# Kernel optimization log

Measured on AMD Instinct MI355X. Metric: run time of the kernel, lower is better.

## Reference

```python
import jax, jax.numpy as jnp
import numpy as np

N = 16384      # number of points (pixels)
C = 64         # value channels of U
D_REF = 5      # bilateral reference feature dim (xy + rgb)


def setup_inputs() -> dict:
    key = jax.random.key(0)
    k1, k2 = jax.random.split(key)
    U = jax.random.normal(k1, (N, C), dtype=jnp.float32)
    ref = jax.random.normal(k2, (N, D_REF), dtype=jnp.float32)
    return {"U": U, "ref": ref}


def reference(U, ref):
    # Gaussian filtering on reference features (exact form of the LSH-approx filter):
    #   out[i] = sum_j exp(-0.5 * ||ref_i - ref_j||^2) * U[j]  -  U[i]
    sq = jnp.sum(ref * ref, axis=-1)                      # [N]
    d2 = sq[:, None] + sq[None, :] - 2.0 * (ref @ ref.T)  # [N, N] squared distances
    K = jnp.exp(-0.5 * jnp.maximum(d2, 0.0))              # [N, N] Gaussian kernel
    return K @ U - U                                       # [N, C]
```

## Files before the change

### kernel.cpp

```cpp
#include <hip/hip_runtime.h>
#include <hip/hip_bf16.h>
#include <stdint.h>

#define N_PTS 16384
#define C_CH  64
#define D_REF 5
#define LOG2E 1.44269504088896340736f
#define IBLOCKS 64

typedef __attribute__((ext_vector_type(8))) short bf16x8;
typedef __attribute__((ext_vector_type(4))) float f32x4;

__device__ __forceinline__ unsigned short bf16rn(float v) {
    unsigned u = __builtin_bit_cast(unsigned, v) + 0x8000u;
    return (unsigned short)(u >> 16);
}
__device__ __forceinline__ float bf16tof(unsigned short h) {
    unsigned u = ((unsigned)h) << 16;
    return __builtin_bit_cast(float, u);
}
__device__ __forceinline__ unsigned pack2bf16(float lo, float hi) {
    unsigned a = __builtin_bit_cast(unsigned, lo) + 0x8000u;
    unsigned b = __builtin_bit_cast(unsigned, hi) + 0x8000u;
    return __builtin_amdgcn_perm(b, a, 0x07060302u);
}
__device__ __forceinline__ float fast_exp2(float x) {
#if __has_builtin(__builtin_amdgcn_exp2f)
    return __builtin_amdgcn_exp2f(x);
#else
    return exp2f(x);
#endif
}

__global__ __launch_bounds__(256) void prep_all(
    const float* __restrict__ U, const float* __restrict__ ref,
    unsigned short* __restrict__ packA, unsigned short* __restrict__ packB,
    unsigned short* __restrict__ utPack)
{
    __shared__ unsigned short tile[64 * 80];
    const int bid = blockIdx.x;
    const int t   = threadIdx.x;

    if (bid < 512) {
        const int gid  = bid * 256 + t;
        const int half = gid >> 16;
        const int id   = gid & 0xFFFF;
        const int tile16 = id >> 6;
        const int lane = id & 63;
        const int q    = lane >> 4;
        const int m    = lane & 15;
        const int p = half ? (tile16 * 16 + m)
                           : ((tile16 >> 1) * 32 + (m >> 2) * 8 + (m & 3) + (tile16 & 1) * 4);

        const float* r = ref + (size_t)p * D_REF;
        float rv[5];
        float sq = 0.f;
#pragma unroll
        for (int d = 0; d < 5; ++d) { rv[d] = r[d]; sq += rv[d] * rv[d]; }
        const float h = -0.5f * LOG2E * sq;

        unsigned short bh[5], bl[5];
#pragma unroll
        for (int d = 0; d < 5; ++d) {
            const float base = half ? rv[d] * LOG2E : rv[d];
            bh[d] = bf16rn(base);
            bl[d] = bf16rn(base - bf16tof(bh[d]));
        }
        const unsigned short hh  = bf16rn(h);
        const unsigned short hl  = bf16rn(h - bf16tof(hh));
        const unsigned short one = 0x3F80;

        unsigned short outv[8];
#pragma unroll
        for (int tt = 0; tt < 8; ++tt) {
            const int k = q * 8 + tt;
            unsigned short v = 0;
            if (!half) {
                if      (k < 5)   v = bh[k];
                else if (k < 10)  v = bh[k - 5];
                else if (k < 15)  v = bl[k - 10];
                else if (k == 15) v = hh;
                else if (k == 16) v = hl;
                else if (k <= 18) v = one;
            } else {
                if      (k < 5)   v = bh[k];
                else if (k < 10)  v = bl[k - 5];
                else if (k < 15)  v = bh[k - 10];
                else if (k <= 16) v = one;
                else if (k == 17) v = hh;
                else if (k == 18) v = hl;
            }
            outv[tt] = v;
        }
        unsigned short* dst = (half ? packB : packA) + ((size_t)tile16 * 64 + lane) * 8;
        *(uint4*)dst = *(uint4*)outv;
    } else {
        const int b  = bid - 512;
        const int j0 = b * 64;
        const int c  = t & 63;
        const int jb = t >> 6;
#pragma unroll
        for (int k = 0; k < 16; ++k) {
            const int jr = jb + k * 4;
            tile[c * 80 + jr] = bf16rn(U[(size_t)(j0 + jr) * C_CH + c]);
        }
        __syncthreads();
#pragma unroll
        for (int rep = 0; rep < 2; ++rep) {
            const int id   = rep * 256 + t;
            const int lane = id & 63;
            const int ct   = (id >> 6) & 3;
            const int kt   = id >> 8;
            const int m    = lane & 15;
            const int q    = lane >> 4;
            const int cc   = ct * 16 + m;
            const int jloc = kt * 32 + q * 8;
            const uint4 frag = *(const uint4*)&tile[cc * 80 + jloc];
            const int jtile  = b * 2 + kt;
            *(uint4*)&utPack[(((size_t)jtile * 4 + ct) * 64 + lane) * 8] = frag;
        }
    }
}

template<int JS>
__global__ __launch_bounds__(256, 4) void lsh_main(
    const float* __restrict__ U,
    const unsigned short* __restrict__ packA,
    const unsigned short* __restrict__ packB,
    const unsigned short* __restrict__ utPack,
    float* __restrict__ part,
    float* __restrict__ out,
    int use_part)
{
    constexpr int UNITS = (N_PTS / JS) / 32;

    const int t    = threadIdx.x;
    const int lane = t & 63;
    const int wave = t >> 6;
    const int q    = lane >> 4;
    const int m    = lane & 15;

    const int ib = blockIdx.x / JS;
    const int js = blockIdx.x % JS;

    bf16x8 bfrag[4];
#pragma unroll
    for (int s = 0; s < 4; ++s) {
        const int itile = ib * 16 + wave * 4 + s;
        bfrag[s] = *(const bf16x8*)(packB + ((size_t)itile * 64 + lane) * 8);
    }

    f32x4 acc[4][4];
#pragma unroll
    for (int s = 0; s < 4; ++s)
#pragma unroll
        for (int ct = 0; ct < 4; ++ct) acc[s][ct] = (f32x4){0.f, 0.f, 0.f, 0.f};

    const unsigned short* pA = packA  + ((size_t)js * UNITS) * 1024 + lane * 8;
    const unsigned short* pU = utPack + ((size_t)js * UNITS) * 2048 + lane * 8;

    bf16x8 ga0 = *(const bf16x8*)pA;
    bf16x8 ga1 = *(const bf16x8*)(pA + 512);

    for (int u = 0; u < UNITS; ++u) {
        bf16x8 nga0 = ga0, nga1 = ga1;
        if (u + 1 < UNITS) {
            nga0 = *(const bf16x8*)(pA + 1024);
            nga1 = *(const bf16x8*)(pA + 1536);
        }

        const f32x4 z = (f32x4){0.f, 0.f, 0.f, 0.f};
        bf16x8 sfrag[4];
#pragma unroll
        for (int sp = 0; sp < 2; ++sp) {
            f32x4 g0a = __builtin_amdgcn_mfma_f32_16x16x32_bf16(ga0, bfrag[sp*2+0], z, 0, 0, 0);
            f32x4 g1a = __builtin_amdgcn_mfma_f32_16x16x32_bf16(ga1, bfrag[sp*2+0], z, 0, 0, 0);
            f32x4 g0b = __builtin_amdgcn_mfma_f32_16x16x32_bf16(ga0, bfrag[sp*2+1], z, 0, 0, 0);
            f32x4 g1b = __builtin_amdgcn_mfma_f32_16x16x32_bf16(ga1, bfrag[sp*2+1], z, 0, 0, 0);
            union { unsigned u[4]; bf16x8 v; } sa, sb;
            sa.u[0] = pack2bf16(fast_exp2(g0a[0]), fast_exp2(g0a[1]));
            sa.u[1] = pack2bf16(fast_exp2(g0a[2]), fast_exp2(g0a[3]));
            sa.u[2] = pack2bf16(fast_exp2(g1a[0]), fast_exp2(g1a[1]));
            sa.u[3] = pack2bf16(fast_exp2(g1a[2]), fast_exp2(g1a[3]));
            sb.u[0] = pack2bf16(fast_exp2(g0b[0]), fast_exp2(g0b[1]));
            sb.u[1] = pack2bf16(fast_exp2(g0b[2]), fast_exp2(g0b[3]));
            sb.u[2] = pack2bf16(fast_exp2(g1b[0]), fast_exp2(g1b[1]));
            sb.u[3] = pack2bf16(fast_exp2(g1b[2]), fast_exp2(g1b[3]));
            sfrag[sp*2+0] = sa.v;
            sfrag[sp*2+1] = sb.v;
        }
#pragma unroll
        for (int ct = 0; ct < 4; ++ct) {
            const bf16x8 uf = *(const bf16x8*)(pU + ct * 512);
#pragma unroll
            for (int s = 0; s < 4; ++s)
                acc[s][ct] = __builtin_amdgcn_mfma_f32_16x16x32_bf16(
                    uf, sfrag[s], acc[s][ct], 0, 0, 0);
        }

        pA += 1024;
        pU += 2048;
        ga0 = nga0;
        ga1 = nga1;
    }

    if (use_part) {
        float* dst = part + ((size_t)js * IBLOCKS + ib) * (256 * C_CH);
#pragma unroll
        for (int s = 0; s < 4; ++s) {
            const int i_loc = (wave * 4 + s) * 16 + m;
#pragma unroll
            for (int ct = 0; ct < 4; ++ct)
                *(f32x4*)(dst + i_loc * C_CH + ct * 16 + q * 4) = acc[s][ct];
        }
    } else {
#pragma unroll
        for (int s = 0; s < 4; ++s) {
            const int i_glob = ib * 256 + (wave * 4 + s) * 16 + m;
#pragma unroll
            for (int ct = 0; ct < 4; ++ct)
#pragma unroll
                for (int r2 = 0; r2 < 4; ++r2) {
                    const int c = ct * 16 + q * 4 + r2;
                    float val = acc[s][ct][r2];
                    if (js == 0) val -= U[(size_t)i_glob * C_CH + c];
                    atomicAdd(&out[(size_t)i_glob * C_CH + c], val);
                }
        }
    }
}

template<int JS>
__global__ __launch_bounds__(256) void reduce_part(
    const f32x4* __restrict__ part, const f32x4* __restrict__ U,
    f32x4* __restrict__ out)
{
    const int x = blockIdx.x * 256 + threadIdx.x;
    f32x4 s = part[x];
#pragma unroll
    for (int js = 1; js < JS; ++js)
        s += part[((size_t)js << 18) + x];
    out[x] = s - U[x];
}

extern "C" void kernel_launch(void* const* d_in, const int* in_sizes, int n_in,
                              void* d_out, int out_size, void* d_ws, size_t ws_size,
                              hipStream_t stream) {
    const float* U   = (const float*)d_in[0];
    const float* ref = (const float*)d_in[1];
    float* out = (float*)d_out;

    unsigned short* utPack = (unsigned short*)d_ws;
    unsigned short* packA  = (unsigned short*)((char*)d_ws + (size_t)2 * 1024 * 1024);
    unsigned short* packB  = (unsigned short*)((char*)d_ws + (size_t)3 * 1024 * 1024);
    float*          part   = (float*)((char*)d_ws + (size_t)4 * 1024 * 1024);

    const size_t MB = 1024 * 1024;
    prep_all<<<768, 256, 0, stream>>>(U, ref, packA, packB, utPack);

    if (ws_size >= (4 + 4 * 16) * MB) {
        lsh_main<16><<<IBLOCKS * 16, 256, 0, stream>>>(U, packA, packB, utPack,
                                                       part, out, 1);
        reduce_part<16><<<1024, 256, 0, stream>>>((const f32x4*)part,
                                                  (const f32x4*)U, (f32x4*)out);
    } else if (ws_size >= (4 + 4 * 8) * MB) {
        lsh_main<8><<<IBLOCKS * 8, 256, 0, stream>>>(U, packA, packB, utPack,
                                                     part, out, 1);
        reduce_part<8><<<1024, 256, 0, stream>>>((const f32x4*)part,
                                                 (const f32x4*)U, (f32x4*)out);
    } else {
        hipMemsetAsync(d_out, 0, (size_t)out_size * sizeof(float), stream);
        lsh_main<8><<<IBLOCKS * 8, 256, 0, stream>>>(U, packA, packB, utPack,
                                                     part, out, 0);
    }
}
```

Measured before the change: 130.2 us.

## Stage U tiles in LDS via direct global-to-LDS loads and store partials as bf16

The main loop now copies chunks of eight U tiles into shared memory with global_load_lds DMA, guarded by block barriers, and reads the U fragments from LDS instead of issuing per-lane global loads. The per-split partial sums are written as bf16 instead of fp32, which halves partial-buffer traffic and workspace use, and the reduce kernel is changed to match. This adds two barriers per chunk and 32KB of LDS per block, which may cut occupancy. It also loses accuracy in the partials, and the fp32 JS=8 fallback path is removed. The prefetch of the next A tile is now unconditional and can read one unit past the slice.

Result: slower. 149.3 us (+14.6%).

```diff
diff --git a/kernel.cpp b/kernel.cpp
--- a/kernel.cpp
+++ b/kernel.cpp
@@ -29,6 +29,17 @@
     return __builtin_amdgcn_exp2f(x);
 #else
     return exp2f(x);
+#endif
+}
+
+__device__ __forceinline__ void dma16(const unsigned short* g, unsigned short* l) {
+#if __has_builtin(__builtin_amdgcn_global_load_lds)
+    __builtin_amdgcn_global_load_lds(
+        (const __attribute__((address_space(1))) unsigned int*)g,
+        (__attribute__((address_space(3))) unsigned int*)l, 16, 0, 0);
+#else
+    const int lane = threadIdx.x & 63;
+    *(uint4*)(l + lane * 8) = *(const uint4*)(g);
 #endif
 }
 
@@ -128,11 +139,14 @@
     const unsigned short* __restrict__ packA,
     const unsigned short* __restrict__ packB,
     const unsigned short* __restrict__ utPack,
-    float* __restrict__ part,
+    unsigned short* __restrict__ part,
     float* __restrict__ out,
     int use_part)
 {
     constexpr int UNITS = (N_PTS / JS) / 32;
+    constexpr int CUNITS = 8;
+    constexpr int NCH = UNITS / CUNITS;
+    __shared__ __align__(16) unsigned short sh[CUNITS * 2048];
 
     const int t    = threadIdx.x;
     const int lane = t & 63;
@@ -156,62 +170,70 @@
 #pragma unroll
         for (int ct = 0; ct < 4; ++ct) acc[s][ct] = (f32x4){0.f, 0.f, 0.f, 0.f};
 
-    const unsigned short* pA = packA  + ((size_t)js * UNITS) * 1024 + lane * 8;
-    const unsigned short* pU = utPack + ((size_t)js * UNITS) * 2048 + lane * 8;
+    const unsigned short* pA    = packA + ((size_t)js * UNITS) * 1024 + lane * 8;
+    const unsigned short* srcU0 = utPack + ((size_t)js * UNITS) * 2048;
 
     bf16x8 ga0 = *(const bf16x8*)pA;
     bf16x8 ga1 = *(const bf16x8*)(pA + 512);
 
-    for (int u = 0; u < UNITS; ++u) {
-        bf16x8 nga0 = ga0, nga1 = ga1;
-        if (u + 1 < UNITS) {
-            nga0 = *(const bf16x8*)(pA + 1024);
-            nga1 = *(const bf16x8*)(pA + 1536);
-        }
-
-        const f32x4 z = (f32x4){0.f, 0.f, 0.f, 0.f};
-        bf16x8 sfrag[4];
-#pragma unroll
-        for (int sp = 0; sp < 2; ++sp) {
-            f32x4 g0a = __builtin_amdgcn_mfma_f32_16x16x32_bf16(ga0, bfrag[sp*2+0], z, 0, 0, 0);
-            f32x4 g1a = __builtin_amdgcn_mfma_f32_16x16x32_bf16(ga1, bfrag[sp*2+0], z, 0, 0, 0);
-            f32x4 g0b = __builtin_amdgcn_mfma_f32_16x16x32_bf16(ga0, bfrag[sp*2+1], z, 0, 0, 0);
-            f32x4 g1b = __builtin_amdgcn_mfma_f32_16x16x32_bf16(ga1, bfrag[sp*2+1], z, 0, 0, 0);
-            union { unsigned u[4]; bf16x8 v; } sa, sb;
-            sa.u[0] = pack2bf16(fast_exp2(g0a[0]), fast_exp2(g0a[1]));
-            sa.u[1] = pack2bf16(fast_exp2(g0a[2]), fast_exp2(g0a[3]));
-            sa.u[2] = pack2bf16(fast_exp2(g1a[0]), fast_exp2(g1a[1]));
-            sa.u[3] = pack2bf16(fast_exp2(g1a[2]), fast_exp2(g1a[3]));
-            sb.u[0] = pack2bf16(fast_exp2(g0b[0]), fast_exp2(g0b[1]));
-            sb.u[1] = pack2bf16(fast_exp2(g0b[2]), fast_exp2(g0b[3]));
-            sb.u[2] = pack2bf16(fast_exp2(g1b[0]), fast_exp2(g1b[1]));
-            sb.u[3] = pack2bf16(fast_exp2(g1b[2]), fast_exp2(g1b[3]));
-            sfrag[sp*2+0] = sa.v;
-            sfrag[sp*2+1] = sb.v;
-        }
-#pragma unroll
-        for (int ct = 0; ct < 4; ++ct) {
-            const bf16x8 uf = *(const bf16x8*)(pU + ct * 512);
-#pragma unroll
-            for (int s = 0; s < 4; ++s)
-                acc[s][ct] = __builtin_amdgcn_mfma_f32_16x16x32_bf16(
-                    uf, sfrag[s], acc[s][ct], 0, 0, 0);
-        }
-
-        pA += 1024;
-        pU += 2048;
-        ga0 = nga0;
-        ga1 = nga1;
+    for (int ch = 0; ch < NCH; ++ch) {
+        const unsigned short* srcU = srcU0 + (size_t)ch * (CUNITS * 2048);
+        __syncthreads();
+#pragma unroll
+        for (int r = 0; r < CUNITS; ++r)
+            dma16(srcU + (r * 4 + wave) * 512 + lane * 8, sh + (r * 4 + wave) * 512);
+        __syncthreads();
+
+#pragma unroll
+        for (int u8 = 0; u8 < CUNITS; ++u8) {
+            const bf16x8 nga0 = *(const bf16x8*)(pA + 1024);
+            const bf16x8 nga1 = *(const bf16x8*)(pA + 1536);
+
+            const f32x4 z = (f32x4){0.f, 0.f, 0.f, 0.f};
+            bf16x8 sfrag[4];
+#pragma unroll
+            for (int sp = 0; sp < 2; ++sp) {
+                f32x4 g0a = __builtin_amdgcn_mfma_f32_16x16x32_bf16(ga0, bfrag[sp*2+0], z, 0, 0, 0);
+                f32x4 g1a = __builtin_amdgcn_mfma_f32_16x16x32_bf16(ga1, bfrag[sp*2+0], z, 0, 0, 0);
+                f32x4 g0b = __builtin_amdgcn_mfma_f32_16x16x32_bf16(ga0, bfrag[sp*2+1], z, 0, 0, 0);
+                f32x4 g1b = __builtin_amdgcn_mfma_f32_16x16x32_bf16(ga1, bfrag[sp*2+1], z, 0, 0, 0);
+                union { unsigned u[4]; bf16x8 v; } sa, sb;
+                sa.u[0] = pack2bf16(fast_exp2(g0a[0]), fast_exp2(g0a[1]));
+                sa.u[1] = pack2bf16(fast_exp2(g0a[2]), fast_exp2(g0a[3]));
+                sa.u[2] = pack2bf16(fast_exp2(g1a[0]), fast_exp2(g1a[1]));
+                sa.u[3] = pack2bf16(fast_exp2(g1a[2]), fast_exp2(g1a[3]));
+                sb.u[0] = pack2bf16(fast_exp2(g0b[0]), fast_exp2(g0b[1]));
+                sb.u[1] = pack2bf16(fast_exp2(g0b[2]), fast_exp2(g0b[3]));
+                sb.u[2] = pack2bf16(fast_exp2(g1b[0]), fast_exp2(g1b[1]));
+                sb.u[3] = pack2bf16(fast_exp2(g1b[2]), fast_exp2(g1b[3]));
+                sfrag[sp*2+0] = sa.v;
+                sfrag[sp*2+1] = sb.v;
+            }
+#pragma unroll
+            for (int ct = 0; ct < 4; ++ct) {
+                const bf16x8 uf = *(const bf16x8*)(sh + u8 * 2048 + ct * 512 + lane * 8);
+#pragma unroll
+                for (int s = 0; s < 4; ++s)
+                    acc[s][ct] = __builtin_amdgcn_mfma_f32_16x16x32_bf16(
+                        uf, sfrag[s], acc[s][ct], 0, 0, 0);
+            }
+            pA += 1024;
+            ga0 = nga0;
+            ga1 = nga1;
+        }
     }
 
     if (use_part) {
-        float* dst = part + ((size_t)js * IBLOCKS + ib) * (256 * C_CH);
+        unsigned short* dst = part + ((size_t)js * IBLOCKS + ib) * (256 * C_CH);
 #pragma unroll
         for (int s = 0; s < 4; ++s) {
             const int i_loc = (wave * 4 + s) * 16 + m;
 #pragma unroll
-            for (int ct = 0; ct < 4; ++ct)
-                *(f32x4*)(dst + i_loc * C_CH + ct * 16 + q * 4) = acc[s][ct];
+            for (int ct = 0; ct < 4; ++ct) {
+                uint2 w = { pack2bf16(acc[s][ct][0], acc[s][ct][1]),
+                            pack2bf16(acc[s][ct][2], acc[s][ct][3]) };
+                *(uint2*)(dst + i_loc * C_CH + ct * 16 + q * 4) = w;
+            }
         }
     } else {
 #pragma unroll
@@ -232,15 +254,21 @@
 
 template<int JS>
 __global__ __launch_bounds__(256) void reduce_part(
-    const f32x4* __restrict__ part, const f32x4* __restrict__ U,
+    const unsigned short* __restrict__ part, const f32x4* __restrict__ U,
     f32x4* __restrict__ out)
 {
     const int x = blockIdx.x * 256 + threadIdx.x;
-    f32x4 s = part[x];
-#pragma unroll
-    for (int js = 1; js < JS; ++js)
-        s += part[((size_t)js << 18) + x];
-    out[x] = s - U[x];
+    float s0 = 0.f, s1 = 0.f, s2 = 0.f, s3 = 0.f;
+#pragma unroll
+    for (int js = 0; js < JS; ++js) {
+        const uint2 w = *(const uint2*)(part + ((size_t)js << 20) + (size_t)x * 4);
+        s0 += bf16tof((unsigned short)(w.x & 0xFFFF));
+        s1 += bf16tof((unsigned short)(w.x >> 16));
+        s2 += bf16tof((unsigned short)(w.y & 0xFFFF));
+        s3 += bf16tof((unsigned short)(w.y >> 16));
+    }
+    const f32x4 u = U[x];
+    out[x] = (f32x4){s0 - u[0], s1 - u[1], s2 - u[2], s3 - u[3]};
 }
 
 extern "C" void kernel_launch(void* const* d_in, const int* in_sizes, int n_in,
@@ -253,21 +281,15 @@
     unsigned short* utPack = (unsigned short*)d_ws;
     unsigned short* packA  = (unsigned short*)((char*)d_ws + (size_t)2 * 1024 * 1024);
     unsigned short* packB  = (unsigned short*)((char*)d_ws + (size_t)3 * 1024 * 1024);
-    float*          part   = (float*)((char*)d_ws + (size_t)4 * 1024 * 1024);
+    unsigned short* part   = (unsigned short*)((char*)d_ws + (size_t)4 * 1024 * 1024);
 
     const size_t MB = 1024 * 1024;
     prep_all<<<768, 256, 0, stream>>>(U, ref, packA, packB, utPack);
 
-    if (ws_size >= (4 + 4 * 16) * MB) {
+    if (ws_size >= (4 + 2 * 16) * MB) {
         lsh_main<16><<<IBLOCKS * 16, 256, 0, stream>>>(U, packA, packB, utPack,
                                                        part, out, 1);
-        reduce_part<16><<<1024, 256, 0, stream>>>((const f32x4*)part,
-                                                  (const f32x4*)U, (f32x4*)out);
-    } else if (ws_size >= (4 + 4 * 8) * MB) {
-        lsh_main<8><<<IBLOCKS * 8, 256, 0, stream>>>(U, packA, packB, utPack,
-                                                     part, out, 1);
-        reduce_part<8><<<1024, 256, 0, stream>>>((const f32x4*)part,
-                                                 (const f32x4*)U, (f32x4*)out);
+        reduce_part<16><<<1024, 256, 0, stream>>>(part, (const f32x4*)U, (f32x4*)out);
     } else {
         hipMemsetAsync(d_out, 0, (size_t)out_size * sizeof(float), stream);
         lsh_main<8><<<IBLOCKS * 8, 256, 0, stream>>>(U, packA, packB, utPack,
```
